# Performance work log

Hardware: AMD Instinct MI355X
Metric: run time of the kernel (lower is better)

Reference implementation:

```python
import jax, jax.numpy as jnp
import numpy as np

NUM_CAPSULE = 10
DIM_CAPSULE = 16
ROUTINGS = 3
EPS = 1e-7  # K.epsilon()


def squash(x, axis=-1):
    sq_norm = jnp.sum(jnp.square(x), axis=axis, keepdims=True) + EPS
    coeff = jnp.sqrt(sq_norm) / (1.0 + sq_norm)
    return coeff * x


def setup_inputs() -> dict:
    key = jax.random.key(0)
    k1, k2 = jax.random.split(key)
    B, I, Din = 64, 4096, 128
    u_vecs = jax.random.normal(k1, (B, I, Din), dtype=jnp.float32)
    # glorot-ish scale for the capsule kernel (flattened conv1d kernel of size 1)
    W = jax.random.normal(k2, (Din, NUM_CAPSULE * DIM_CAPSULE), dtype=jnp.float32) * 0.06
    return {"u_vecs": u_vecs, "W": W}


def reference(u_vecs, W):
    B, I, Din = u_vecs.shape
    N, D = NUM_CAPSULE, DIM_CAPSULE
    # conv1d with kernel size 1 == per-position matmul
    u_hat = jnp.einsum('bid,dk->bik', u_vecs, W)          # [B, I, N*D]
    u_hat = u_hat.reshape(B, I, N, D).transpose(0, 2, 1, 3)  # [B, N, I, D]

    b = jnp.zeros((B, N, I), dtype=u_hat.dtype)
    outputs = None
    for i in range(ROUTINGS):
        c = jax.nn.softmax(b, axis=1)                      # softmax over num_capsule
        s = jnp.einsum('bni,bnid->bnd', c, u_hat)          # weighted sum over input caps
        outputs = squash(s)                                # [B, N, D]
        if i < ROUTINGS - 1:
            b = jnp.einsum('bnd,bnid->bni', outputs, u_hat)  # agreement logits
    return outputs
```

## Files before the change

kernel.cpp:

```cpp
#include <hip/hip_runtime.h>
#include <hip/hip_bf16.h>
#include <math.h>

#define NCAP 10
#define DCAP 16
#define DIN  128
#define NPOS 4096
#define NB   64

typedef short short8 __attribute__((ext_vector_type(8)));
typedef float floatx4 __attribute__((ext_vector_type(4)));

__device__ inline float bflo(unsigned v) { return __uint_as_float(v << 16); }
__device__ inline float bfhi(unsigned v) { return __uint_as_float(v & 0xFFFF0000u); }
__device__ inline unsigned short f2bf(float f) {
    unsigned u = __float_as_uint(f);
    return (unsigned short)((u + 0x7FFFu + ((u >> 16) & 1u)) >> 16);
}
__device__ inline float bf2f(unsigned short h) { return __uint_as_float(((unsigned)h) << 16); }


__global__ __launch_bounds__(256) void wprep(const float* __restrict__ W,
                                             uint4* __restrict__ WTg) {
    const int cid = blockIdx.x * 256 + threadIdx.x;
    if (cid >= 2560) return;
    const int row = cid >> 4;
    const int csn = cid & 15;
    const int kc = csn ^ (row & 15);
    unsigned p[4];
    #pragma unroll
    for (int e = 0; e < 4; ++e) {
        const float a = W[(kc * 8 + e * 2) * 160 + row];
        const float b = W[(kc * 8 + e * 2 + 1) * 160 + row];
        p[e] = (unsigned)f2bf(a) | ((unsigned)f2bf(b) << 16);
    }
    WTg[cid] = make_uint4(p[0], p[1], p[2], p[3]);
}

__global__ __launch_bounds__(256) void gemm_uhat(const float* __restrict__ u,
                                                 const uint4* __restrict__ WTg,
                                                 uint2* __restrict__ uf2,
                                                 float* __restrict__ partial) {
    const int b = blockIdx.x;
    const int blk = blockIdx.y;
    const int t = threadIdx.x;
    const int l = t & 63;
    const int wv = __builtin_amdgcn_readfirstlane(t >> 6);

    const float4* u4g = (const float4*)u;
    const short8* wt8g = (const short8*)WTg;

    float cs[4][8];
    #pragma unroll
    for (int kk = 0; kk < 4; ++kk)
        #pragma unroll
        for (int e = 0; e < 8; ++e) cs[kk][e] = 0.f;

    short8 ubf[2][4];
    #pragma unroll
    for (int mt = 0; mt < 2; ++mt) {
        const size_t row = (size_t)b * NPOS + blk * 128 + mt * 64 + wv * 16 + (l & 15);
        #pragma unroll
        for (int kk = 0; kk < 4; ++kk) {
            const float4 x0 = u4g[row * 32 + kk * 8 + (l >> 4) * 2];
            const float4 x1 = u4g[row * 32 + kk * 8 + (l >> 4) * 2 + 1];
            cs[kk][0] += x0.x; cs[kk][1] += x0.y; cs[kk][2] += x0.z; cs[kk][3] += x0.w;
            cs[kk][4] += x1.x; cs[kk][5] += x1.y; cs[kk][6] += x1.z; cs[kk][7] += x1.w;
            short8 a;
            a[0] = (short)f2bf(x0.x); a[1] = (short)f2bf(x0.y);
            a[2] = (short)f2bf(x0.z); a[3] = (short)f2bf(x0.w);
            a[4] = (short)f2bf(x1.x); a[5] = (short)f2bf(x1.y);
            a[6] = (short)f2bf(x1.z); a[7] = (short)f2bf(x1.w);
            ubf[mt][kk] = a;
        }
    }

    #pragma unroll 2
    for (int n = 0; n < 10; ++n) {
        short8 wf[4];
        #pragma unroll
        for (int kk = 0; kk < 4; ++kk)
            wf[kk] = wt8g[(n * 16 + (l & 15)) * 16 + ((kk * 4 + (l >> 4)) ^ (l & 15))];
        #pragma unroll
        for (int mt = 0; mt < 2; ++mt) {
            floatx4 a = {0.f, 0.f, 0.f, 0.f};
            #pragma unroll
            for (int kk = 0; kk < 4; ++kk)
                a = __builtin_amdgcn_mfma_f32_16x16x32_bf16(wf[kk], ubf[mt][kk], a, 0, 0, 0);
            uint2 pk;
            pk.x = (unsigned)f2bf(a[0]) | ((unsigned)f2bf(a[1]) << 16);
            pk.y = (unsigned)f2bf(a[2]) | ((unsigned)f2bf(a[3]) << 16);
            const size_t cell = ((size_t)(b * 64 + blk * 2 + mt) * 4 + wv) * 10;
            uf2[(cell + n) * 64 + l] = pk;
        }
    }

    __shared__ float csbuf[4][128];
    #pragma unroll
    for (int kk = 0; kk < 4; ++kk)
        #pragma unroll
        for (int e = 0; e < 8; ++e) {
            float v = cs[kk][e];
            v += __shfl_xor(v, 1); v += __shfl_xor(v, 2);
            v += __shfl_xor(v, 4); v += __shfl_xor(v, 8);
            cs[kk][e] = v;
        }
    if ((l & 15) == 0) {
        #pragma unroll
        for (int kk = 0; kk < 4; ++kk)
            #pragma unroll
            for (int e = 0; e < 8; ++e)
                csbuf[wv][kk * 32 + (l >> 4) * 8 + e] = cs[kk][e];
    }
    __syncthreads();
    if (t < 128)
        partial[(size_t)(b * 32 + blk) * 128 + t] =
            csbuf[0][t] + csbuf[1][t] + csbuf[2][t] + csbuf[3][t];
}

__global__ __launch_bounds__(128) void small0(const float* __restrict__ partial,
                                              const float* __restrict__ W,
                                              float* __restrict__ vbuf) {
    const int b = blockIdx.x / NCAP;
    const int n = blockIdx.x % NCAP;
    const int t = threadIdx.x;
    __shared__ float xv[DIN];
    float a = 0.f;
    #pragma unroll 8
    for (int c = 0; c < 32; ++c)
        a += partial[(size_t)(b * 32 + c) * DIN + t];
    xv[t] = a;
    __syncthreads();
    if (t < DCAP) {
        float sv = 0.f;
        for (int d = 0; d < DIN; ++d)
            sv = fmaf(xv[d], W[d * 160 + n * DCAP + t], sv);
        sv *= 0.1f;
        float nq = sv * sv;
        #pragma unroll
        for (int mm = 8; mm >= 1; mm >>= 1) nq += __shfl_xor(nq, mm, 16);
        nq += 1e-7f;
        vbuf[(size_t)(b * NCAP + n) * DCAP + t] = sv * sqrtf(nq) / (1.0f + nq);
    }
}

__global__ __launch_bounds__(256) void route_uf(const uint2* __restrict__ uf2,
                                                const float* __restrict__ vbuf,
                                                float* __restrict__ pws) {
    const int b = blockIdx.x;
    const int g = blockIdx.y;
    const int t = threadIdx.x;
    const int l = t & 63;
    const int w = __builtin_amdgcn_readfirstlane(t >> 6);

    __shared__ __align__(16) short tls[64 * 168];
    __shared__ float lgp[4][64][10];
    __shared__ float csm[64][10];

    const size_t base = (size_t)(b * 64 + g) * 2560 + (size_t)w * 640;
    const int pos = w * 16 + (l & 15);
    const int d0 = (l >> 4) * 4;
    #pragma unroll
    for (int n = 0; n < 10; ++n) {
        const uint2 q = uf2[base + n * 64 + l];
        *(uint2*)&tls[pos * 168 + n * 16 + d0] = q;
    }
    __syncthreads();

    #pragma unroll
    for (int n = 0; n < 10; ++n) {
        const uint2 uu = *(const uint2*)&tls[l * 168 + n * 16 + w * 4];
        const float4 vq = *(const float4*)&vbuf[(size_t)(b * 10 + n) * 16 + w * 4];
        lgp[w][l][n] = bflo(uu.x) * vq.x + bfhi(uu.x) * vq.y +
                       bflo(uu.y) * vq.z + bfhi(uu.y) * vq.w;
    }
    __syncthreads();

    float c[10];
    float m = -1e30f;
    #pragma unroll
    for (int n = 0; n < 10; ++n) {
        c[n] = lgp[0][l][n] + lgp[1][l][n] + lgp[2][l][n] + lgp[3][l][n];
        m = fmaxf(m, c[n]);
    }
    float ssum = 0.f;
    #pragma unroll
    for (int n = 0; n < 10; ++n) { c[n] = __expf(c[n] - m); ssum += c[n]; }
    const float inv = 1.0f / ssum;
    if (w == 0) {
        #pragma unroll
        for (int n = 0; n < 10; ++n) csm[l][n] = c[n] * inv;
    }
    __syncthreads();

    if (t < 160) {
        const int n = t >> 4;
        float acc = 0.f;
        #pragma unroll 8
        for (int p = 0; p < 64; ++p)
            acc = fmaf(csm[p][n], bf2f((unsigned short)tls[p * 168 + t]), acc);
        pws[(size_t)(b * 64 + g) * 160 + t] = acc;
    }
}

__global__ __launch_bounds__(256) void smallv(const float* __restrict__ pws,
                                              float* __restrict__ dst) {
    const int b = blockIdx.x;
    const int t = threadIdx.x;
    if (t >= 160) return;
    float a = 0.f;
    #pragma unroll 8
    for (int c = 0; c < 64; ++c)
        a += pws[(size_t)(b * 64 + c) * 160 + t];
    float nq = a * a;
    #pragma unroll
    for (int mm = 8; mm >= 1; mm >>= 1) nq += __shfl_xor(nq, mm, 16);
    nq += 1e-7f;
    dst[(size_t)b * 160 + t] = a * sqrtf(nq) / (1.0f + nq);
}


__global__ __launch_bounds__(256) void caps_sum(const float* __restrict__ u,
                                                float* __restrict__ partial) {
    const int b = blockIdx.x;
    const int chunk = blockIdx.y;
    const int t = threadIdx.x;
    const int v4 = t & 31;
    const int prow = t >> 5;
    const float4* up = (const float4*)u;
    const size_t posbase = (size_t)b * NPOS + chunk * 256;
    float4 acc = make_float4(0.f, 0.f, 0.f, 0.f);
    #pragma unroll 8
    for (int j = 0; j < 32; ++j) {
        float4 x = up[(posbase + prow + j * 8) * 32 + v4];
        acc.x += x.x; acc.y += x.y; acc.z += x.z; acc.w += x.w;
    }
    __shared__ float4 red[8][32];
    red[prow][v4] = acc;
    __syncthreads();
    if (t < 32) {
        float4 s = red[0][t];
        #pragma unroll
        for (int r = 1; r < 8; ++r) {
            s.x += red[r][t].x; s.y += red[r][t].y;
            s.z += red[r][t].z; s.w += red[r][t].w;
        }
        ((float4*)partial)[((size_t)b * 16 + chunk) * 32 + t] = s;
    }
}

template <int MODE>
__global__ __launch_bounds__(128) void caps_small(const float* __restrict__ src,
                                                  const float* __restrict__ W,
                                                  float* __restrict__ dst) {
    const int b = blockIdx.x / NCAP;
    const int n = blockIdx.x % NCAP;
    const int t = threadIdx.x;
    __shared__ float xv[DIN];
    __shared__ float vv[DCAP];
    float a = 0.f;
    if (MODE == 0) {
        #pragma unroll 4
        for (int c = 0; c < 16; ++c) a += src[(size_t)(b * 16 + c) * DIN + t];
    } else {
        #pragma unroll 4
        for (int c = 0; c < 16; ++c) a += src[((size_t)(b * 16 + c) * NCAP + n) * DIN + t];
    }
    xv[t] = a;
    __syncthreads();
    if (t < DCAP) {
        float sv = 0.f;
        for (int d = 0; d < DIN; ++d) sv = fmaf(xv[d], W[d * 160 + n * DCAP + t], sv);
        if (MODE == 0) sv *= 0.1f;
        float nq = sv * sv;
        #pragma unroll
        for (int mm = 8; mm >= 1; mm >>= 1) nq += __shfl_xor(nq, mm, 16);
        nq += 1e-7f;
        const float v = sv * sqrtf(nq) / (1.0f + nq);
        if (MODE == 2) dst[(size_t)(b * NCAP + n) * DCAP + t] = v;
        else vv[t] = v;
    }
    if (MODE != 2) {
        __syncthreads();
        float wd = 0.f;
        #pragma unroll
        for (int dd = 0; dd < DCAP; ++dd)
            wd = fmaf(W[t * 160 + n * DCAP + dd], vv[dd], wd);
        dst[(size_t)(b * NCAP + n) * DIN + t] = wd;
    }
}

__global__ __launch_bounds__(256, 3) void caps_route(const float* __restrict__ u,
                                                     const float* __restrict__ wsrc,
                                                     float* __restrict__ pdst) {
    const int b = blockIdx.x;
    const int tile = blockIdx.y;
    const int t = threadIdx.x;
    const int lane = t & 63;
    const int wv = __builtin_amdgcn_readfirstlane(t >> 6);
    __shared__ float4 tl4[64 * 32];
    __shared__ float lgp[4][64][11];
    float* tlf = (float*)tl4;
    const float4* wq4 = (const float4*)(wsrc + (size_t)b * (NCAP * DIN));
    float acc0[NCAP], acc1[NCAP];
    #pragma unroll
    for (int n = 0; n < NCAP; ++n) { acc0[n] = 0.f; acc1[n] = 0.f; }
    for (int s = 0; s < 4; ++s) {
        __syncthreads();
        const float4* src4 = (const float4*)u + ((size_t)b * NPOS + tile * 256 + s * 64) * 32;
        #pragma unroll
        for (int i = 0; i < 8; ++i) {
            const int q = t + i * 256;
            const int r = q >> 5, c = q & 31;
            tl4[r * 32 + (c ^ (r & 7))] = src4[q];
        }
        __syncthreads();
        float lg[NCAP];
        #pragma unroll
        for (int n = 0; n < NCAP; ++n) lg[n] = 0.f;
        #pragma unroll
        for (int j = 0; j < 8; ++j) {
            const float4 u4 = tl4[lane * 32 + wv * 8 + (j ^ (lane & 7))];
            #pragma unroll
            for (int n = 0; n < NCAP; ++n) {
                const float4 w4 = wq4[n * 32 + wv * 8 + j];
                lg[n] = fmaf(u4.x, w4.x, fmaf(u4.y, w4.y,
                        fmaf(u4.z, w4.z, fmaf(u4.w, w4.w, lg[n]))));
            }
        }
        #pragma unroll
        for (int n = 0; n < NCAP; ++n) lgp[wv][lane][n] = lg[n];
        __syncthreads();
        float c[NCAP];
        float m = -1e30f;
        #pragma unroll
        for (int n = 0; n < NCAP; ++n) {
            c[n] = lgp[0][lane][n] + lgp[1][lane][n] + lgp[2][lane][n] + lgp[3][lane][n];
            m = fmaxf(m, c[n]);
        }
        float ssum = 0.f;
        #pragma unroll
        for (int n = 0; n < NCAP; ++n) { c[n] = __expf(c[n] - m); ssum += c[n]; }
        const float inv = 1.0f / ssum;
        #pragma unroll
        for (int n = 0; n < NCAP; ++n) c[n] *= inv;
        const int col0 = lane >> 2, word = lane & 3;
        #pragma unroll
        for (int i = 0; i < 16; ++i) {
            const int p = wv * 16 + i;
            const int ca = col0 ^ (p & 7);
            const float u0 = tlf[(p * 32 + ca) * 4 + word];
            const float u1 = tlf[(p * 32 + ca + 16) * 4 + word];
            #pragma unroll
            for (int n = 0; n < NCAP; ++n) {
                const float cp = __int_as_float(
                    __builtin_amdgcn_readlane(__float_as_int(c[n]), p));
                acc0[n] = fmaf(cp, u0, acc0[n]);
                acc1[n] = fmaf(cp, u1, acc1[n]);
            }
        }
    }
    __syncthreads();
    float* red = tlf;
    #pragma unroll
    for (int n = 0; n < NCAP; ++n) {
        red[(wv * NCAP + n) * DIN + lane]      = acc0[n];
        red[(wv * NCAP + n) * DIN + lane + 64] = acc1[n];
    }
    __syncthreads();
    float* pb = pdst + (size_t)(b * 16 + tile) * (NCAP * DIN);
    for (int k = t; k < NCAP * DIN; k += 256)
        pb[k] = red[k] + red[1280 + k] + red[2560 + k] + red[3840 + k];
}

extern "C" void kernel_launch(void* const* d_in, const int* in_sizes, int n_in,
                              void* d_out, int out_size, void* d_ws, size_t ws_size,
                              hipStream_t stream) {
    const float* u = (const float*)d_in[0];
    const float* W = (const float*)d_in[1];
    float* out = (float*)d_out;
    char* wsb = (char*)d_ws;

    if (ws_size >= 86679552ull) {
        float* partial = (float*)wsb;
        float* pws     = (float*)wsb;
        float* vbuf    = (float*)(wsb + 2621440);
        uint4* WTg     = (uint4*)(wsb + 2662400);
        uint2* uf2     = (uint2*)(wsb + 2703360);

        wprep<<<10, 256, 0, stream>>>(W, WTg);
        gemm_uhat<<<dim3(NB, 32), 256, 0, stream>>>(u, WTg, uf2, partial);
        small0<<<NB * NCAP, 128, 0, stream>>>(partial, W, vbuf);
        route_uf<<<dim3(NB, 64), 256, 0, stream>>>(uf2, vbuf, pws);
        smallv<<<NB, 256, 0, stream>>>(pws, vbuf);
        route_uf<<<dim3(NB, 64), 256, 0, stream>>>(uf2, vbuf, pws);
        smallv<<<NB, 256, 0, stream>>>(pws, out);
    } else {
        float* partial = (float*)wsb;
        float* wbuf    = (float*)wsb + 131072;
        float* pws32   = (float*)wsb + 212992;
        caps_sum<<<dim3(NB, 16), 256, 0, stream>>>(u, partial);
        caps_small<0><<<NB * NCAP, 128, 0, stream>>>(partial, W, wbuf);
        caps_route<<<dim3(NB, 16), 256, 0, stream>>>(u, wbuf, pws32);
        caps_small<1><<<NB * NCAP, 128, 0, stream>>>(pws32, W, wbuf);
        caps_route<<<dim3(NB, 16), 256, 0, stream>>>(u, wbuf, pws32);
        caps_small<2><<<NB * NCAP, 128, 0, stream>>>(pws32, W, out);
    }
}
```

Before: 115.5 us.

## Stage u tiles through swizzled LDS for coalesced loads and simpler column sums

Each wave now loads its 32 rows of u with fully coalesced float4 reads, where a half-wave covers one full 512-byte row. It converts them to bf16 and writes them into a per-wave XOR-swizzled LDS tile, then reads back the MFMA B-fragments from LDS. The column-sum reduction drops from many shuffle stages to a single xor-32 shuffle. Output cell indexing is remapped so each wave owns two consecutive 16-row subtiles. The cost is 32KB of extra LDS per block and an LDS round trip, which may lower occupancy.

```diff
diff --git a/kernel.cpp b/kernel.cpp
--- a/kernel.cpp
+++ b/kernel.cpp
@@ -47,34 +47,43 @@
     const int l = t & 63;
     const int wv = __builtin_amdgcn_readfirstlane(t >> 6);
 
+    __shared__ __align__(16) char ust[4][8192];
+    __shared__ float csbuf[4][128];
+
     const float4* u4g = (const float4*)u;
     const short8* wt8g = (const short8*)WTg;
-
-    float cs[4][8];
-    #pragma unroll
-    for (int kk = 0; kk < 4; ++kk)
-        #pragma unroll
-        for (int e = 0; e < 8; ++e) cs[kk][e] = 0.f;
-
-    short8 ubf[2][4];
-    #pragma unroll
-    for (int mt = 0; mt < 2; ++mt) {
-        const size_t row = (size_t)b * NPOS + blk * 128 + mt * 64 + wv * 16 + (l & 15);
-        #pragma unroll
-        for (int kk = 0; kk < 4; ++kk) {
-            const float4 x0 = u4g[row * 32 + kk * 8 + (l >> 4) * 2];
-            const float4 x1 = u4g[row * 32 + kk * 8 + (l >> 4) * 2 + 1];
-            cs[kk][0] += x0.x; cs[kk][1] += x0.y; cs[kk][2] += x0.z; cs[kk][3] += x0.w;
-            cs[kk][4] += x1.x; cs[kk][5] += x1.y; cs[kk][6] += x1.z; cs[kk][7] += x1.w;
-            short8 a;
-            a[0] = (short)f2bf(x0.x); a[1] = (short)f2bf(x0.y);
-            a[2] = (short)f2bf(x0.z); a[3] = (short)f2bf(x0.w);
-            a[4] = (short)f2bf(x1.x); a[5] = (short)f2bf(x1.y);
-            a[6] = (short)f2bf(x1.z); a[7] = (short)f2bf(x1.w);
-            ubf[mt][kk] = a;
-        }
-    }
-
+    char* myst = ust[wv];
+
+    const int col4 = l & 31;
+    const int par  = l >> 5;
+    const int kcs  = col4 >> 1;
+    const int hh   = col4 & 1;
+    float cs4[4] = {0.f, 0.f, 0.f, 0.f};
+
+    #pragma unroll
+    for (int r = 0; r < 2; ++r) {
+        #pragma unroll
+        for (int i = 0; i < 8; ++i) {
+            const int pl = r * 16 + i * 2 + par;
+            const size_t grow = (size_t)b * NPOS + blk * 128 + wv * 32 + pl;
+            const float4 x = u4g[grow * 32 + col4];
+            cs4[0] += x.x; cs4[1] += x.y; cs4[2] += x.z; cs4[3] += x.w;
+            uint2 pk;
+            pk.x = (unsigned)f2bf(x.x) | ((unsigned)f2bf(x.y) << 16);
+            pk.y = (unsigned)f2bf(x.z) | ((unsigned)f2bf(x.w) << 16);
+            *(uint2*)&myst[pl * 256 + ((kcs ^ (pl & 15)) << 4) + hh * 8] = pk;
+        }
+    }
+
+    short8 bfr[2][4];
+    #pragma unroll
+    for (int mt = 0; mt < 2; ++mt)
+        #pragma unroll
+        for (int kk = 0; kk < 4; ++kk)
+            bfr[mt][kk] = *(const short8*)&myst[(mt * 16 + (l & 15)) * 256 +
+                              (((kk * 4 + (l >> 4)) ^ (l & 15)) << 4)];
+
+    const int sub = 2 * wv;
     #pragma unroll 2
     for (int n = 0; n < 10; ++n) {
         short8 wf[4];
@@ -86,32 +95,20 @@
             floatx4 a = {0.f, 0.f, 0.f, 0.f};
             #pragma unroll
             for (int kk = 0; kk < 4; ++kk)
-                a = __builtin_amdgcn_mfma_f32_16x16x32_bf16(wf[kk], ubf[mt][kk], a, 0, 0, 0);
+                a = __builtin_amdgcn_mfma_f32_16x16x32_bf16(wf[kk], bfr[mt][kk], a, 0, 0, 0);
             uint2 pk;
             pk.x = (unsigned)f2bf(a[0]) | ((unsigned)f2bf(a[1]) << 16);
             pk.y = (unsigned)f2bf(a[2]) | ((unsigned)f2bf(a[3]) << 16);
-            const size_t cell = ((size_t)(b * 64 + blk * 2 + mt) * 4 + wv) * 10;
+            const int sm = sub + mt;
+            const size_t cell = ((size_t)(b * 64 + blk * 2 + (sm >> 2)) * 4 + (sm & 3)) * 10;
             uf2[(cell + n) * 64 + l] = pk;
         }
     }
 
-    __shared__ float csbuf[4][128];
-    #pragma unroll
-    for (int kk = 0; kk < 4; ++kk)
-        #pragma unroll
-        for (int e = 0; e < 8; ++e) {
-            float v = cs[kk][e];
-            v += __shfl_xor(v, 1); v += __shfl_xor(v, 2);
-            v += __shfl_xor(v, 4); v += __shfl_xor(v, 8);
-            cs[kk][e] = v;
-        }
-    if ((l & 15) == 0) {
-        #pragma unroll
-        for (int kk = 0; kk < 4; ++kk)
-            #pragma unroll
-            for (int e = 0; e < 8; ++e)
-                csbuf[wv][kk * 32 + (l >> 4) * 8 + e] = cs[kk][e];
-    }
+    #pragma unroll
+    for (int e = 0; e < 4; ++e) cs4[e] += __shfl_xor(cs4[e], 32);
+    if (l < 32)
+        *(float4*)&csbuf[wv][l * 4] = make_float4(cs4[0], cs4[1], cs4[2], cs4[3]);
     __syncthreads();
     if (t < 128)
         partial[(size_t)(b * 32 + blk) * 128 + t] =
```

After: 108.0 us. 6.5% less time.
